# Optimization experiments

Measured on AMD Instinct MI355X. Metric: run time of the kernel, lower is better.

## Reference

```python
import jax, jax.numpy as jnp
import numpy as np

N_NODES = 50000
N_EDGES = 800000
IN_CH = 128
HID = 64
OUT_CH = 10
N_GRAPHS = 512


def setup_inputs() -> dict:
    key = jax.random.key(0)
    ks = jax.random.split(key, 16)
    x = jax.random.normal(ks[0], (N_NODES, IN_CH), dtype=jnp.float32)
    edge_index = jax.random.randint(ks[1], (2, N_EDGES), 0, N_NODES, dtype=jnp.int64)
    batch = jnp.sort(jax.random.randint(ks[2], (N_NODES,), 0, N_GRAPHS, dtype=jnp.int64))
    def lin(k, fan_in, fan_out):
        bound = 1.0 / np.sqrt(fan_in)
        kw, kb = jax.random.split(k)
        w = jax.random.uniform(kw, (fan_in, fan_out), minval=-bound, maxval=bound, dtype=jnp.float32)
        b = jax.random.uniform(kb, (fan_out,), minval=-bound, maxval=bound, dtype=jnp.float32)
        return w, b
    w0a, b0a = lin(ks[3], IN_CH, HID)
    w0b, b0b = lin(ks[4], HID, HID)
    w1a, b1a = lin(ks[5], HID, HID)
    w1b, b1b = lin(ks[6], HID, HID)
    fcw, fcb = lin(ks[7], HID, OUT_CH)
    eps0 = jnp.zeros((), dtype=jnp.float32)  # train_eps=True, init 0
    eps1 = jnp.zeros((), dtype=jnp.float32)
    return {"x": x, "edge_index": edge_index, "batch": batch,
            "eps0": eps0, "w0a": w0a, "b0a": b0a, "w0b": w0b, "b0b": b0b,
            "eps1": eps1, "w1a": w1a, "b1a": b1a, "w1b": w1b, "b1b": b1b,
            "fcw": fcw, "fcb": fcb}


def _gin_layer(x, src, dst, eps, wa, ba, wb, bb):
    # sum-aggregate neighbor messages: agg[i] = sum_{(j->i) in E} x[j]
    agg = jax.ops.segment_sum(x[src], dst, num_segments=N_NODES)
    h = (1.0 + eps) * x + agg
    h = jax.nn.relu(h @ wa + ba)
    h = jax.nn.relu(h @ wb + bb)  # MLP ends in ReLU; outer F.relu is a no-op
    return h


def reference(x, edge_index, batch, eps0, w0a, b0a, w0b, b0b,
              eps1, w1a, b1a, w1b, b1b, fcw, fcb):
    src, dst = edge_index[0], edge_index[1]
    h = _gin_layer(x, src, dst, eps0, w0a, b0a, w0b, b0b)
    # dropout skipped (inference)
    h = _gin_layer(h, src, dst, eps1, w1a, b1a, w1b, b1b)
    pooled = jax.ops.segment_sum(h, batch, num_segments=N_GRAPHS)  # [G, HID]
    logits = pooled @ fcw + fcb
    return jax.nn.log_softmax(logits, axis=1)
```

## Files before the change

kernel.cpp:

```cpp
#include <hip/hip_runtime.h>
#include <math.h>

#define IN_CH 128
#define HID 64
#define OUT_CH 10

typedef unsigned int uint32;
typedef unsigned char u8;
typedef unsigned short bf16u;
typedef __attribute__((ext_vector_type(8))) short bf16x8;
typedef __attribute__((ext_vector_type(4))) float f32x4;
typedef __attribute__((ext_vector_type(2))) float f32x2;

static __device__ inline bf16u f2bf(float f) {
    uint32 u = __float_as_uint(f);
    u += 0x7fff + ((u >> 16) & 1);
    return (bf16u)(u >> 16);
}
static __device__ inline uint32 pack2(float a, float b) {
    return (uint32)f2bf(a) | ((uint32)f2bf(b) << 16);
}
static __device__ inline u8 f2fp8(float v) {
    uint32 p = __builtin_amdgcn_cvt_pk_fp8_f32(v, v, 0, false);
    return (u8)(p & 0xff);
}
static __device__ inline void acc_fp8x4(uint32 u, float& a0, float& a1,
                                        float& a2, float& a3) {
    f32x2 lo = __builtin_amdgcn_cvt_pk_f32_fp8((int)u, false);
    f32x2 hi = __builtin_amdgcn_cvt_pk_f32_fp8((int)u, true);
    a0 += lo.x; a1 += lo.y; a2 += hi.x; a3 += hi.y;
}

static __device__ inline void gather_group(
    const uint32* __restrict__ y8, const int* __restrict__ col,
    int rs, int re, int c2,
    float& a0, float& a1, float& a2, float& a3)
{
    int j = rs;
    for (; j + 4 <= re; j += 4) {
        int s0 = col[j];
        int s1 = col[j + 1];
        int s2 = col[j + 2];
        int s3 = col[j + 3];
        uint32 u0 = y8[s0 * 16 + c2];
        uint32 u1 = y8[s1 * 16 + c2];
        uint32 u2 = y8[s2 * 16 + c2];
        uint32 u3 = y8[s3 * 16 + c2];
        acc_fp8x4(u0, a0, a1, a2, a3);
        acc_fp8x4(u1, a0, a1, a2, a3);
        acc_fp8x4(u2, a0, a1, a2, a3);
        acc_fp8x4(u3, a0, a1, a2, a3);
    }
    for (; j < re; ++j) {
        uint32 u = y8[col[j] * 16 + c2];
        acc_fp8x4(u, a0, a1, a2, a3);
    }
}

__global__ __launch_bounds__(256, 6) void k_pre(
    const int* __restrict__ dst, int* __restrict__ cnt, int* __restrict__ pos,
    const float4* __restrict__ x4, const float* __restrict__ w,
    u8* __restrict__ y, int N, int E)
{
    int gt = blockIdx.x * 256 + threadIdx.x;
    for (int e = gt; e < E; e += gridDim.x * 256)
        pos[e] = atomicAdd(&cnt[dst[e]], 1);

    __shared__ __align__(16) uint32 t32[16 * 68];
    int tid = threadIdx.x;
    int wid = tid >> 6, lane = tid & 63;
    int quad = lane >> 4, n15 = lane & 15;
    int mycol = wid * 16 + n15;
    bf16x8 fb[4];
    #pragma unroll
    for (int s = 0; s < 4; s++)
        #pragma unroll
        for (int j = 0; j < 8; j++)
            fb[s][j] = (short)f2bf(w[(s * 32 + quad * 8 + j) * HID + mycol]);
    int snode = tid >> 4, sk = tid & 15;
    for (long g0 = (long)blockIdx.x * 16; g0 < N; g0 += (long)gridDim.x * 16) {
        long node = g0 + snode;
        if (node < N) {
            float4 v0 = x4[node * 32 + sk * 2];
            float4 v1 = x4[node * 32 + sk * 2 + 1];
            uint32 p[4] = {pack2(v0.x, v0.y), pack2(v0.z, v0.w),
                           pack2(v1.x, v1.y), pack2(v1.z, v1.w)};
            *(uint4*)((char*)t32 + snode * 272 + sk * 16) = *(uint4*)p;
        }
        __syncthreads();
        f32x4 acc = {0.f, 0.f, 0.f, 0.f};
        #pragma unroll
        for (int s = 0; s < 4; s++) {
            bf16x8 a = *(const bf16x8*)((const char*)t32 + n15 * 272 + s * 64 + quad * 16);
            acc = __builtin_amdgcn_mfma_f32_16x16x32_bf16(a, fb[s], acc, 0, 0, 0);
        }
        #pragma unroll
        for (int r = 0; r < 4; r++) {
            long n = g0 + quad * 4 + r;
            if (n < N) y[n * HID + mycol] = f2fp8(acc[r]);
        }
        __syncthreads();
    }
}

__global__ __launch_bounds__(256) void k_scan(
    const int* __restrict__ cnt, int* __restrict__ row_ptr,
    int* __restrict__ partials, int* __restrict__ counter, int N, int E, int nch)
{
    __shared__ int red[256];
    int tid = threadIdx.x;
    int bid = blockIdx.x;
    long base = (long)bid * 1024 + tid * 4;
    int v[4]; int s = 0;
    #pragma unroll
    for (int i = 0; i < 4; i++) {
        long idx = base + i;
        v[i] = (idx < N) ? cnt[idx] : 0;
        s += v[i];
    }
    red[tid] = s;
    __syncthreads();
    for (int off = 1; off < 256; off <<= 1) {
        int t = (tid >= off) ? red[tid - off] : 0;
        __syncthreads();
        red[tid] += t;
        __syncthreads();
    }
    int myexcl = red[tid] - s;
    if (tid == 255) {
        __hip_atomic_store(&partials[bid], red[255], __ATOMIC_RELEASE,
                           __HIP_MEMORY_SCOPE_AGENT);
        atomicAdd(counter, 1);
    }
    if (tid == 0) {
        while (__hip_atomic_load(counter, __ATOMIC_ACQUIRE,
                                 __HIP_MEMORY_SCOPE_AGENT) < nch) { }
    }
    __syncthreads();
    int off = 0;
    for (int i = tid; i < bid; i += 256)
        off += __hip_atomic_load(&partials[i], __ATOMIC_RELAXED,
                                 __HIP_MEMORY_SCOPE_AGENT);
    __syncthreads();
    red[tid] = off;
    __syncthreads();
    for (int o = 128; o; o >>= 1) {
        if (tid < o) red[tid] += red[tid + o];
        __syncthreads();
    }
    int run = red[0] + myexcl;
    #pragma unroll
    for (int i = 0; i < 4; i++) {
        long idx = base + i;
        if (idx < N) row_ptr[idx] = run;
        run += v[i];
    }
    if (bid == 0 && tid == 0) row_ptr[N] = E;
}

__global__ __launch_bounds__(256) void k_place(
    const int* __restrict__ src, const int* __restrict__ dst,
    const int* __restrict__ row_ptr, const int* __restrict__ pos,
    int* __restrict__ col, int E)
{
    int e = blockIdx.x * 256 + threadIdx.x;
    if (e >= E) return;
    col[row_ptr[dst[e]] + pos[e]] = src[e];
}

__global__ __launch_bounds__(256, 6) void k_agg0f(
    const uint32* __restrict__ y8, const int* __restrict__ row_ptr,
    const int* __restrict__ col, const float* __restrict__ epsp,
    const float* __restrict__ ba, const float* __restrict__ wb,
    const float* __restrict__ bb, const float* __restrict__ w1a,
    u8* __restrict__ y1, int N)
{
    __shared__ __align__(16) uint32 t32[16 * 36];
    __shared__ __align__(16) uint32 h32[16 * 36];
    int tid = threadIdx.x;
    int wid = tid >> 6, lane = tid & 63;
    int c2 = lane & 15, h = lane >> 4;
    int quad = lane >> 4, n15 = lane & 15;
    int n0 = wid * 4;
    int mycol = wid * 16 + n15;
    float e = 1.f + epsp[0];
    float4 bav = ((const float4*)ba)[c2];
    float bbv = bb[mycol];
    bf16x8 fb[2], f1[2];
    #pragma unroll
    for (int s = 0; s < 2; s++)
        #pragma unroll
        for (int j = 0; j < 8; j++) {
            fb[s][j] = (short)f2bf(wb[(s * 32 + quad * 8 + j) * HID + mycol]);
            f1[s][j] = (short)f2bf(w1a[(s * 32 + quad * 8 + j) * HID + mycol]);
        }
    for (long g0 = (long)blockIdx.x * 16; g0 < N; g0 += (long)gridDim.x * 16) {
        long node = g0 + n0 + h;
        if (node < N) {
            int rs = row_ptr[node], re = row_ptr[node + 1];
            uint32 us = y8[node * 16 + c2];
            float a0 = 0.f, a1 = 0.f, a2 = 0.f, a3 = 0.f;
            gather_group(y8, col, rs, re, c2, a0, a1, a2, a3);
            f32x2 lo = __builtin_amdgcn_cvt_pk_f32_fp8((int)us, false);
            f32x2 hi = __builtin_amdgcn_cvt_pk_f32_fp8((int)us, true);
            a0 = fmaf(e, lo.x, a0); a1 = fmaf(e, lo.y, a1);
            a2 = fmaf(e, hi.x, a2); a3 = fmaf(e, hi.y, a3);
            t32[(n0 + h) * 36 + 2 * c2]     = pack2(fmaxf(a0 + bav.x, 0.f),
                                                    fmaxf(a1 + bav.y, 0.f));
            t32[(n0 + h) * 36 + 2 * c2 + 1] = pack2(fmaxf(a2 + bav.z, 0.f),
                                                    fmaxf(a3 + bav.w, 0.f));
        }
        __syncthreads();
        f32x4 acc = {bbv, bbv, bbv, bbv};
        {
            bf16x8 a0 = *(const bf16x8*)((const char*)t32 + n15 * 144 + quad * 16);
            bf16x8 a1 = *(const bf16x8*)((const char*)t32 + n15 * 144 + 64 + quad * 16);
            acc = __builtin_amdgcn_mfma_f32_16x16x32_bf16(a0, fb[0], acc, 0, 0, 0);
            acc = __builtin_amdgcn_mfma_f32_16x16x32_bf16(a1, fb[1], acc, 0, 0, 0);
        }
        #pragma unroll
        for (int r = 0; r < 4; r++)
            ((short*)h32)[(quad * 4 + r) * 72 + mycol] = (short)f2bf(fmaxf(acc[r], 0.f));
        __syncthreads();
        f32x4 acc2 = {0.f, 0.f, 0.f, 0.f};
        {
            bf16x8 a0 = *(const bf16x8*)((const char*)h32 + n15 * 144 + quad * 16);
            bf16x8 a1 = *(const bf16x8*)((const char*)h32 + n15 * 144 + 64 + quad * 16);
            acc2 = __builtin_amdgcn_mfma_f32_16x16x32_bf16(a0, f1[0], acc2, 0, 0, 0);
            acc2 = __builtin_amdgcn_mfma_f32_16x16x32_bf16(a1, f1[1], acc2, 0, 0, 0);
        }
        #pragma unroll
        for (int r = 0; r < 4; r++) {
            long n = g0 + quad * 4 + r;
            if (n < N) y1[n * HID + mycol] = f2fp8(acc2[r]);
        }
    }
}

__global__ __launch_bounds__(256, 6) void k_agg1(
    const uint32* __restrict__ y8, const int* __restrict__ row_ptr,
    const int* __restrict__ col, const float* __restrict__ epsp,
    const float* __restrict__ ba, const float* __restrict__ wb,
    const float* __restrict__ bb, const int* __restrict__ batch,
    float* __restrict__ pooled, int N)
{
    __shared__ __align__(16) uint32 t32[16 * 36];
    int tid = threadIdx.x;
    int wid = tid >> 6, lane = tid & 63;
    int c2 = lane & 15, h = lane >> 4;
    int quad = lane >> 4, n15 = lane & 15;
    int n0 = wid * 4;
    int mycol = wid * 16 + n15;
    float e = 1.f + epsp[0];
    float4 bav = ((const float4*)ba)[c2];
    float bbv = bb[mycol];
    bf16x8 fb[2];
    #pragma unroll
    for (int s = 0; s < 2; s++)
        #pragma unroll
        for (int j = 0; j < 8; j++)
            fb[s][j] = (short)f2bf(wb[(s * 32 + quad * 8 + j) * HID + mycol]);
    for (long g0 = (long)blockIdx.x * 16; g0 < N; g0 += (long)gridDim.x * 16) {
        long node = g0 + n0 + h;
        if (node < N) {
            int rs = row_ptr[node], re = row_ptr[node + 1];
            uint32 us = y8[node * 16 + c2];
            float a0 = 0.f, a1 = 0.f, a2 = 0.f, a3 = 0.f;
            gather_group(y8, col, rs, re, c2, a0, a1, a2, a3);
            f32x2 lo = __builtin_amdgcn_cvt_pk_f32_fp8((int)us, false);
            f32x2 hi = __builtin_amdgcn_cvt_pk_f32_fp8((int)us, true);
            a0 = fmaf(e, lo.x, a0); a1 = fmaf(e, lo.y, a1);
            a2 = fmaf(e, hi.x, a2); a3 = fmaf(e, hi.y, a3);
            t32[(n0 + h) * 36 + 2 * c2]     = pack2(fmaxf(a0 + bav.x, 0.f),
                                                    fmaxf(a1 + bav.y, 0.f));
            t32[(n0 + h) * 36 + 2 * c2 + 1] = pack2(fmaxf(a2 + bav.z, 0.f),
                                                    fmaxf(a3 + bav.w, 0.f));
        }
        __syncthreads();
        f32x4 acc = {bbv, bbv, bbv, bbv};
        {
            bf16x8 a0 = *(const bf16x8*)((const char*)t32 + n15 * 144 + quad * 16);
            bf16x8 a1 = *(const bf16x8*)((const char*)t32 + n15 * 144 + 64 + quad * 16);
            acc = __builtin_amdgcn_mfma_f32_16x16x32_bf16(a0, fb[0], acc, 0, 0, 0);
            acc = __builtin_amdgcn_mfma_f32_16x16x32_bf16(a1, fb[1], acc, 0, 0, 0);
        }
        float rv[4];
        #pragma unroll
        for (int r = 0; r < 4; r++) rv[r] = fmaxf(acc[r], 0.f);
        int nv = (int)((N - g0) < 16 ? (N - g0) : 16);
        int bf_ = batch[g0], bl_ = batch[g0 + nv - 1];
        if (bf_ == bl_) {
            float s = 0.f;
            #pragma unroll
            for (int r = 0; r < 4; r++)
                if (quad * 4 + r < nv) s += rv[r];
            s += __shfl_xor(s, 16);
            s += __shfl_xor(s, 32);
            if (quad == 0)
                atomicAdd(&pooled[(long)bf_ * HID + mycol], s);
        } else {
            #pragma unroll
            for (int r = 0; r < 4; r++) {
                long n = g0 + quad * 4 + r;
                if (n < N)
                    atomicAdd(&pooled[(long)batch[n] * HID + mycol], rv[r]);
            }
        }
        __syncthreads();
    }
}

__global__ __launch_bounds__(64) void k_head(
    const float* __restrict__ pooled, const float* __restrict__ fcw,
    const float* __restrict__ fcb, float* __restrict__ out)
{
    int g = blockIdx.x;
    int l = threadIdx.x;
    float logit = -INFINITY;
    if (l < OUT_CH) {
        float acc = fcb[l];
        #pragma unroll
        for (int k = 0; k < HID; k++)
            acc = fmaf(pooled[g * HID + k], fcw[k * OUT_CH + l], acc);
        logit = acc;
    }
    float m = logit;
    #pragma unroll
    for (int off = 32; off; off >>= 1) m = fmaxf(m, __shfl_xor(m, off));
    float ex = (l < OUT_CH) ? expf(logit - m) : 0.0f;
    float s = ex;
    #pragma unroll
    for (int off = 32; off; off >>= 1) s += __shfl_xor(s, off);
    if (l < OUT_CH) out[g * OUT_CH + l] = logit - m - logf(s);
}

extern "C" void kernel_launch(void* const* d_in, const int* in_sizes, int n_in,
                              void* d_out, int out_size, void* d_ws, size_t ws_size,
                              hipStream_t stream) {
    const float* x    = (const float*)d_in[0];
    const int*   ei   = (const int*)d_in[1];
    const int*   batch= (const int*)d_in[2];
    const float* eps0 = (const float*)d_in[3];
    const float* w0a  = (const float*)d_in[4];
    const float* b0a  = (const float*)d_in[5];
    const float* w0b  = (const float*)d_in[6];
    const float* b0b  = (const float*)d_in[7];
    const float* eps1 = (const float*)d_in[8];
    const float* w1a  = (const float*)d_in[9];
    const float* b1a  = (const float*)d_in[10];
    const float* w1b  = (const float*)d_in[11];
    const float* b1b  = (const float*)d_in[12];
    const float* fcw  = (const float*)d_in[13];
    const float* fcb  = (const float*)d_in[14];
    float* out = (float*)d_out;

    const int N = in_sizes[0] / IN_CH;
    const int E = in_sizes[1] / 2;
    const int G = out_size / OUT_CH;
    const int* src = ei;
    const int* dst = ei + E;

    char* ws = (char*)d_ws;
    int*    row_ptr  = (int*)(ws);
    int*    colv     = (int*)(ws + 200064);
    u8*     y0       = (u8*)(ws + 3400064);
    u8*     y1       = (u8*)(ws + 6600064);
    int*    cnt      = (int*)(ws + 9800064);
    int*    counter  = (int*)(ws + 10000064);
    int*    partials = (int*)(ws + 10000128);
    float*  pooled   = (float*)(ws + 10000384);
    int*    pos      = (int*)(ws + 10131456);

    hipMemsetAsync(cnt, 0, 331392, stream);

    int eb = (E + 255) / 256;
    int nb = (N + 31) / 32;
    int nch = (N + 1023) / 1024;
    k_pre<<<nb, 256, 0, stream>>>(dst, cnt, pos, (const float4*)x, w0a, y0, N, E);
    k_scan<<<nch, 256, 0, stream>>>(cnt, row_ptr, partials, counter, N, E, nch);
    k_place<<<eb, 256, 0, stream>>>(src, dst, row_ptr, pos, colv, E);

    k_agg0f<<<nb, 256, 0, stream>>>((const uint32*)y0, row_ptr, colv, eps0,
                                    b0a, w0b, b0b, w1a, y1, N);
    k_agg1<<<nb, 256, 0, stream>>>((const uint32*)y1, row_ptr, colv, eps1,
                                   b1a, w1b, b1b, batch, pooled, N);
    k_head<<<G, 64, 0, stream>>>(pooled, fcw, fcb, out);
}
```

Baseline: 199.0 us.

## Software-pipeline neighbor gathers, split edge counting from dynamic GEMM work queue

The gather loop now preloads eight column indices ahead, so the index loads for the next batch overlap the feature loads of the current one. In k_pre, only the first CBLK blocks perform the edge-degree atomics, and node-group GEMM work is handed out through an atomic work counter so blocks that skip counting pick up more of it. The aggregation kernels' launch-bounds occupancy hint drops from 6 to 4 to leave room for the extra live registers. The work counter shares the memset region, and the deeper prefetch adds register pressure that may lower occupancy.

```diff
diff --git a/kernel.cpp b/kernel.cpp
--- a/kernel.cpp
+++ b/kernel.cpp
@@ -4,6 +4,7 @@
 #define IN_CH 128
 #define HID 64
 #define OUT_CH 10
+#define CBLK 512
 
 typedef unsigned int uint32;
 typedef unsigned char u8;
@@ -33,26 +34,48 @@
 
 static __device__ inline void gather_group(
     const uint32* __restrict__ y8, const int* __restrict__ col,
-    int rs, int re, int c2,
+    int rs, int re, int cc,
     float& a0, float& a1, float& a2, float& a3)
 {
     int j = rs;
-    for (; j + 4 <= re; j += 4) {
-        int s0 = col[j];
-        int s1 = col[j + 1];
-        int s2 = col[j + 2];
-        int s3 = col[j + 3];
-        uint32 u0 = y8[s0 * 16 + c2];
-        uint32 u1 = y8[s1 * 16 + c2];
-        uint32 u2 = y8[s2 * 16 + c2];
-        uint32 u3 = y8[s3 * 16 + c2];
+    if (j + 8 <= re) {
+        int c0 = col[j],     c1 = col[j + 1], c2 = col[j + 2], c3 = col[j + 3],
+            c4 = col[j + 4], c5 = col[j + 5], c6 = col[j + 6], c7 = col[j + 7];
+        j += 8;
+        while (j + 8 <= re) {
+            int n0 = col[j],     n1 = col[j + 1], n2 = col[j + 2], n3 = col[j + 3],
+                n4 = col[j + 4], n5 = col[j + 5], n6 = col[j + 6], n7 = col[j + 7];
+            uint32 u0 = y8[(long)c0 * 16 + cc], u1 = y8[(long)c1 * 16 + cc],
+                   u2 = y8[(long)c2 * 16 + cc], u3 = y8[(long)c3 * 16 + cc],
+                   u4 = y8[(long)c4 * 16 + cc], u5 = y8[(long)c5 * 16 + cc],
+                   u6 = y8[(long)c6 * 16 + cc], u7 = y8[(long)c7 * 16 + cc];
+            acc_fp8x4(u0, a0, a1, a2, a3);
+            acc_fp8x4(u1, a0, a1, a2, a3);
+            acc_fp8x4(u2, a0, a1, a2, a3);
+            acc_fp8x4(u3, a0, a1, a2, a3);
+            acc_fp8x4(u4, a0, a1, a2, a3);
+            acc_fp8x4(u5, a0, a1, a2, a3);
+            acc_fp8x4(u6, a0, a1, a2, a3);
+            acc_fp8x4(u7, a0, a1, a2, a3);
+            c0 = n0; c1 = n1; c2 = n2; c3 = n3;
+            c4 = n4; c5 = n5; c6 = n6; c7 = n7;
+            j += 8;
+        }
+        uint32 u0 = y8[(long)c0 * 16 + cc], u1 = y8[(long)c1 * 16 + cc],
+               u2 = y8[(long)c2 * 16 + cc], u3 = y8[(long)c3 * 16 + cc],
+               u4 = y8[(long)c4 * 16 + cc], u5 = y8[(long)c5 * 16 + cc],
+               u6 = y8[(long)c6 * 16 + cc], u7 = y8[(long)c7 * 16 + cc];
         acc_fp8x4(u0, a0, a1, a2, a3);
         acc_fp8x4(u1, a0, a1, a2, a3);
         acc_fp8x4(u2, a0, a1, a2, a3);
         acc_fp8x4(u3, a0, a1, a2, a3);
+        acc_fp8x4(u4, a0, a1, a2, a3);
+        acc_fp8x4(u5, a0, a1, a2, a3);
+        acc_fp8x4(u6, a0, a1, a2, a3);
+        acc_fp8x4(u7, a0, a1, a2, a3);
     }
     for (; j < re; ++j) {
-        uint32 u = y8[col[j] * 16 + c2];
+        uint32 u = y8[(long)col[j] * 16 + cc];
         acc_fp8x4(u, a0, a1, a2, a3);
     }
 }
@@ -60,14 +83,17 @@
 __global__ __launch_bounds__(256, 6) void k_pre(
     const int* __restrict__ dst, int* __restrict__ cnt, int* __restrict__ pos,
     const float4* __restrict__ x4, const float* __restrict__ w,
-    u8* __restrict__ y, int N, int E)
-{
-    int gt = blockIdx.x * 256 + threadIdx.x;
-    for (int e = gt; e < E; e += gridDim.x * 256)
-        pos[e] = atomicAdd(&cnt[dst[e]], 1);
+    u8* __restrict__ y, int* __restrict__ wctr, int N, int E)
+{
+    int tid = threadIdx.x;
+    int bid = blockIdx.x;
+    if (bid < CBLK) {
+        for (int e = bid * 256 + tid; e < E; e += CBLK * 256)
+            pos[e] = atomicAdd(&cnt[dst[e]], 1);
+    }
 
     __shared__ __align__(16) uint32 t32[16 * 68];
-    int tid = threadIdx.x;
+    __shared__ int sgrp;
     int wid = tid >> 6, lane = tid & 63;
     int quad = lane >> 4, n15 = lane & 15;
     int mycol = wid * 16 + n15;
@@ -78,7 +104,13 @@
         for (int j = 0; j < 8; j++)
             fb[s][j] = (short)f2bf(w[(s * 32 + quad * 8 + j) * HID + mycol]);
     int snode = tid >> 4, sk = tid & 15;
-    for (long g0 = (long)blockIdx.x * 16; g0 < N; g0 += (long)gridDim.x * 16) {
+    int NG = (N + 15) >> 4;
+    while (true) {
+        if (tid == 0) sgrp = atomicAdd(wctr, 1);
+        __syncthreads();
+        int grp = sgrp;
+        if (grp >= NG) break;
+        long g0 = (long)grp * 16;
         long node = g0 + snode;
         if (node < N) {
             float4 v0 = x4[node * 32 + sk * 2];
@@ -168,7 +200,7 @@
     col[row_ptr[dst[e]] + pos[e]] = src[e];
 }
 
-__global__ __launch_bounds__(256, 6) void k_agg0f(
+__global__ __launch_bounds__(256, 4) void k_agg0f(
     const uint32* __restrict__ y8, const int* __restrict__ row_ptr,
     const int* __restrict__ col, const float* __restrict__ epsp,
     const float* __restrict__ ba, const float* __restrict__ wb,
@@ -179,12 +211,12 @@
     __shared__ __align__(16) uint32 h32[16 * 36];
     int tid = threadIdx.x;
     int wid = tid >> 6, lane = tid & 63;
-    int c2 = lane & 15, h = lane >> 4;
+    int cc = lane & 15, h = lane >> 4;
     int quad = lane >> 4, n15 = lane & 15;
     int n0 = wid * 4;
     int mycol = wid * 16 + n15;
     float e = 1.f + epsp[0];
-    float4 bav = ((const float4*)ba)[c2];
+    float4 bav = ((const float4*)ba)[cc];
     float bbv = bb[mycol];
     bf16x8 fb[2], f1[2];
     #pragma unroll
@@ -198,16 +230,16 @@
         long node = g0 + n0 + h;
         if (node < N) {
             int rs = row_ptr[node], re = row_ptr[node + 1];
-            uint32 us = y8[node * 16 + c2];
+            uint32 us = y8[node * 16 + cc];
             float a0 = 0.f, a1 = 0.f, a2 = 0.f, a3 = 0.f;
-            gather_group(y8, col, rs, re, c2, a0, a1, a2, a3);
+            gather_group(y8, col, rs, re, cc, a0, a1, a2, a3);
             f32x2 lo = __builtin_amdgcn_cvt_pk_f32_fp8((int)us, false);
             f32x2 hi = __builtin_amdgcn_cvt_pk_f32_fp8((int)us, true);
             a0 = fmaf(e, lo.x, a0); a1 = fmaf(e, lo.y, a1);
             a2 = fmaf(e, hi.x, a2); a3 = fmaf(e, hi.y, a3);
-            t32[(n0 + h) * 36 + 2 * c2]     = pack2(fmaxf(a0 + bav.x, 0.f),
+            t32[(n0 + h) * 36 + 2 * cc]     = pack2(fmaxf(a0 + bav.x, 0.f),
                                                     fmaxf(a1 + bav.y, 0.f));
-            t32[(n0 + h) * 36 + 2 * c2 + 1] = pack2(fmaxf(a2 + bav.z, 0.f),
+            t32[(n0 + h) * 36 + 2 * cc + 1] = pack2(fmaxf(a2 + bav.z, 0.f),
                                                     fmaxf(a3 + bav.w, 0.f));
         }
         __syncthreads();
@@ -237,7 +269,7 @@
     }
 }
 
-__global__ __launch_bounds__(256, 6) void k_agg1(
+__global__ __launch_bounds__(256, 4) void k_agg1(
     const uint32* __restrict__ y8, const int* __restrict__ row_ptr,
     const int* __restrict__ col, const float* __restrict__ epsp,
     const float* __restrict__ ba, const float* __restrict__ wb,
@@ -247,12 +279,12 @@
     __shared__ __align__(16) uint32 t32[16 * 36];
     int tid = threadIdx.x;
     int wid = tid >> 6, lane = tid & 63;
-    int c2 = lane & 15, h = lane >> 4;
+    int cc = lane & 15, h = lane >> 4;
     int quad = lane >> 4, n15 = lane & 15;
     int n0 = wid * 4;
     int mycol = wid * 16 + n15;
     float e = 1.f + epsp[0];
-    float4 bav = ((const float4*)ba)[c2];
+    float4 bav = ((const float4*)ba)[cc];
     float bbv = bb[mycol];
     bf16x8 fb[2];
     #pragma unroll
@@ -264,16 +296,16 @@
         long node = g0 + n0 + h;
         if (node < N) {
             int rs = row_ptr[node], re = row_ptr[node + 1];
-            uint32 us = y8[node * 16 + c2];
+            uint32 us = y8[node * 16 + cc];
             float a0 = 0.f, a1 = 0.f, a2 = 0.f, a3 = 0.f;
-            gather_group(y8, col, rs, re, c2, a0, a1, a2, a3);
+            gather_group(y8, col, rs, re, cc, a0, a1, a2, a3);
             f32x2 lo = __builtin_amdgcn_cvt_pk_f32_fp8((int)us, false);
             f32x2 hi = __builtin_amdgcn_cvt_pk_f32_fp8((int)us, true);
             a0 = fmaf(e, lo.x, a0); a1 = fmaf(e, lo.y, a1);
             a2 = fmaf(e, hi.x, a2); a3 = fmaf(e, hi.y, a3);
-            t32[(n0 + h) * 36 + 2 * c2]     = pack2(fmaxf(a0 + bav.x, 0.f),
+            t32[(n0 + h) * 36 + 2 * cc]     = pack2(fmaxf(a0 + bav.x, 0.f),
                                                     fmaxf(a1 + bav.y, 0.f));
-            t32[(n0 + h) * 36 + 2 * c2 + 1] = pack2(fmaxf(a2 + bav.z, 0.f),
+            t32[(n0 + h) * 36 + 2 * cc + 1] = pack2(fmaxf(a2 + bav.z, 0.f),
                                                     fmaxf(a3 + bav.w, 0.f));
         }
         __syncthreads();
@@ -367,6 +399,7 @@
     u8*     y1       = (u8*)(ws + 6600064);
     int*    cnt      = (int*)(ws + 9800064);
     int*    counter  = (int*)(ws + 10000064);
+    int*    wctr     = (int*)(ws + 10000068);
     int*    partials = (int*)(ws + 10000128);
     float*  pooled   = (float*)(ws + 10000384);
     int*    pos      = (int*)(ws + 10131456);
@@ -376,7 +409,8 @@
     int eb = (E + 255) / 256;
     int nb = (N + 31) / 32;
     int nch = (N + 1023) / 1024;
-    k_pre<<<nb, 256, 0, stream>>>(dst, cnt, pos, (const float4*)x, w0a, y0, N, E);
+    k_pre<<<nb, 256, 0, stream>>>(dst, cnt, pos, (const float4*)x, w0a, y0,
+                                  wctr, N, E);
     k_scan<<<nch, 256, 0, stream>>>(cnt, row_ptr, partials, counter, N, E, nch);
     k_place<<<eb, 256, 0, stream>>>(src, dst, row_ptr, pos, colv, E);
 
```

Measured after the change: 238.1 us. 1.2x slower.
